# Kernel optimization log

Measured on AMD Instinct MI355X. Metric: run time of the kernel, lower is better.

## Reference

```python
import jax, jax.numpy as jnp
import numpy as np

B, T, C = 2, 2048, 1024
E, F = 8, 1024        # n_experts, expert ffn dim
FS = 2048             # shared expert ffn dim
TOP_K = 2


def setup_inputs() -> dict:
    key = jax.random.key(0)
    ks = jax.random.split(key, 6)
    s = lambda *d: 1.0 / np.sqrt(d[-1])
    return {
        "hidden_tensor": jax.random.normal(ks[0], (B, T, C), jnp.float32),
        "w_router": jax.random.normal(ks[1], (E, C), jnp.float32) * s(C),
        "w1_stack": jax.random.normal(ks[2], (E, F, C), jnp.float32) * s(C),
        "w2_stack": jax.random.normal(ks[3], (E, C, F), jnp.float32) * s(F),
        "ws1": jax.random.normal(ks[4], (FS, C), jnp.float32) * s(C),
        "ws2": jax.random.normal(ks[5], (C, FS), jnp.float32) * s(FS),
    }


def reference(hidden_tensor, w_router, w1_stack, w2_stack, ws1, ws2):
    Bb, Tt, Cc = hidden_tensor.shape
    x = hidden_tensor.reshape(-1, Cc)                      # (t, C)
    t = x.shape[0]

    # --- router: softmax over experts, top-k, renormalize ---
    logits = x @ w_router.T                                # (t, E)
    probs = jax.nn.softmax(logits, axis=-1)
    expert_weight, expert_idx = jax.lax.top_k(probs, TOP_K)  # (t, k)
    expert_weight = expert_weight / jnp.sum(expert_weight, axis=-1, keepdims=True)

    # --- dispatch: stable sort token-expert pairs by expert id ---
    flat_e = expert_idx.reshape(-1)                        # (t*k,)
    order = jnp.argsort(flat_e, stable=True)
    sorted_e = flat_e[order]
    flat_tok = jnp.repeat(jnp.arange(t), TOP_K)
    sorted_tok = flat_tok[order]
    sorted_w = expert_weight.reshape(-1)[order]

    counts = jnp.bincount(sorted_e, length=E)              # (E,)
    offsets = jnp.concatenate([jnp.zeros((1,), counts.dtype), jnp.cumsum(counts)])
    local_pos = jnp.arange(t * TOP_K) - offsets[sorted_e]  # position within expert bin

    cap = t * TOP_K  # static capacity (>= true cnt_max), padding rows stay zero
    binned = jnp.zeros((E, cap, Cc), x.dtype).at[sorted_e, local_pos].set(x[sorted_tok])

    # --- grouped expert FFN with squared-ReLU ---
    inter = jnp.einsum('ecd,efd->ecf', binned, w1_stack)   # (E, cap, F)
    inter = jnp.square(jax.nn.relu(inter))
    outb = jnp.einsum('ecf,edf->ecd', inter, w2_stack)     # (E, cap, C)

    # --- combine: gather back, weight, scatter-add to tokens ---
    flat_out = outb[sorted_e, local_pos] * sorted_w[:, None]
    moe_out = jnp.zeros((t, Cc), x.dtype).at[sorted_tok].add(flat_out)
    moe_out = moe_out.reshape(Bb, Tt, Cc)

    # --- shared expert on residual (squared-ReLU MLP) ---
    sh = jnp.square(jax.nn.relu(jnp.einsum('btc,fc->btf', hidden_tensor, ws1)))
    shared_out = jnp.einsum('btf,cf->btc', sh, ws2)

    return shared_out + moe_out
```

## Files before the change

### kernel.cpp

```cpp
#include <hip/hip_runtime.h>
#include <math.h>

typedef unsigned short u16;
typedef unsigned int u32;

typedef __attribute__((ext_vector_type(8))) short bf16x8;
typedef __attribute__((ext_vector_type(4))) float f32x4;

__device__ __forceinline__ u16 f2bf(float f) {
  union { float f; u32 u; } v; v.f = f;
  u32 r = v.u + 0x7FFFu + ((v.u >> 16) & 1u);
  return (u16)(r >> 16);
}

typedef const u32 __attribute__((address_space(1)))* gas1_t;
typedef u32 __attribute__((address_space(3)))* las3_t;

__device__ __forceinline__ void gload16(const void* g, void* l) {
  __builtin_amdgcn_global_load_lds((gas1_t)g, (las3_t)l, 16, 0, 0);
}

__global__ __launch_bounds__(256) void convert_weights(
    const float4* __restrict__ w1, const float4* __restrict__ w2,
    const float4* __restrict__ s1, const float4* __restrict__ s2,
    ushort4* __restrict__ o1, ushort4* __restrict__ o2,
    ushort4* __restrict__ o3, ushort4* __restrict__ o4) {
  size_t i = (size_t)blockIdx.x * 256 + threadIdx.x;
  const size_t n1 = 2097152, n2 = 2097152, n3 = 524288;
  float4 v; ushort4* o; size_t j;
  if (i < n1)              { v = w1[i];            o = o1; j = i; }
  else if (i < n1+n2)      { v = w2[i-n1];         o = o2; j = i-n1; }
  else if (i < n1+n2+n3)   { v = s1[i-n1-n2];      o = o3; j = i-n1-n2; }
  else                     { v = s2[i-n1-n2-n3];   o = o4; j = i-n1-n2-n3; }
  ushort4 r; r.x = f2bf(v.x); r.y = f2bf(v.y); r.z = f2bf(v.z); r.w = f2bf(v.w);
  o[j] = r;
}

__global__ __launch_bounds__(256) void router_kernel(
    const float* __restrict__ x, const float* __restrict__ wr,
    u16* __restrict__ xb, int* __restrict__ tokE, float* __restrict__ tokW) {
  const int wv = threadIdx.x >> 6, lane = threadIdx.x & 63;
  const int tok = blockIdx.x * 4 + wv;
  const float4* xp = (const float4*)(x + (size_t)tok * 1024);
  float4 xv[4];
#pragma unroll
  for (int i = 0; i < 4; ++i) xv[i] = xp[i * 64 + lane];
  ushort4* xo = (ushort4*)xb + (size_t)tok * 256;
#pragma unroll
  for (int i = 0; i < 4; ++i) {
    ushort4 o;
    o.x = f2bf(xv[i].x); o.y = f2bf(xv[i].y); o.z = f2bf(xv[i].z); o.w = f2bf(xv[i].w);
    xo[i * 64 + lane] = o;
  }
  float acc[8];
#pragma unroll
  for (int e = 0; e < 8; ++e) acc[e] = 0.f;
#pragma unroll
  for (int e = 0; e < 8; ++e) {
    const float4* wp = (const float4*)(wr + e * 1024);
#pragma unroll
    for (int i = 0; i < 4; ++i) {
      float4 w4 = wp[i * 64 + lane];
      acc[e] += xv[i].x * w4.x + xv[i].y * w4.y + xv[i].z * w4.z + xv[i].w * w4.w;
    }
  }
#pragma unroll
  for (int m = 32; m > 0; m >>= 1)
#pragma unroll
    for (int e = 0; e < 8; ++e) acc[e] += __shfl_xor(acc[e], m, 64);
  if (lane == 0) {
    int e0 = 0;
#pragma unroll
    for (int e = 1; e < 8; ++e) if (acc[e] > acc[e0]) e0 = e;
    int e1 = (e0 == 0) ? 1 : 0;
#pragma unroll
    for (int e = 0; e < 8; ++e) if (e != e0 && acc[e] > acc[e1]) e1 = e;
    float p1 = __expf(acc[e1] - acc[e0]);
    float w1 = p1 / (1.f + p1);
    float w0 = 1.f - w1;
    tokE[tok * 2] = e0; tokE[tok * 2 + 1] = e1;
    tokW[tok * 2] = w0; tokW[tok * 2 + 1] = w1;
  }
}

__global__ __launch_bounds__(256) void plan_kernel(
    const int* __restrict__ tokE, const float* __restrict__ tokW,
    int* __restrict__ tileMeta, int* __restrict__ rowtok,
    float* __restrict__ roww, int* __restrict__ invrow) {
  const int t = threadIdx.x, lane = t & 63, wv = t >> 6;
  int myE[32];
#pragma unroll
  for (int i = 0; i < 32; ++i) myE[i] = tokE[t * 32 + i];
  int lcnt[8] = {};
#pragma unroll
  for (int i = 0; i < 32; ++i) ++lcnt[myE[i]];

  __shared__ int wtot[8][4];
  __shared__ int aoffS[9];
  int excl[8];
#pragma unroll
  for (int e = 0; e < 8; ++e) {
    int v = lcnt[e];
#pragma unroll
    for (int off = 1; off < 64; off <<= 1) {
      int n = __shfl_up(v, (unsigned)off, 64);
      if (lane >= off) v += n;
    }
    if (lane == 63) wtot[e][wv] = v;
    excl[e] = v - lcnt[e];
  }
  __syncthreads();
#pragma unroll
  for (int e = 0; e < 8; ++e)
    for (int w = 0; w < wv; ++w) excl[e] += wtot[e][w];

  if (t == 0) {
    int s = 0, ti = 0;
    for (int e = 0; e < 8; ++e) {
      aoffS[e] = s;
      int cnt = wtot[e][0] + wtot[e][1] + wtot[e][2] + wtot[e][3];
      int tiles = (cnt + 127) >> 7;
      for (int k = 0; k < tiles; ++k) { tileMeta[2 * ti] = e; tileMeta[2 * ti + 1] = s + k * 128; ++ti; }
      s += tiles << 7;
    }
    aoffS[8] = s;
    for (; ti < 72; ++ti) { tileMeta[2 * ti] = -1; tileMeta[2 * ti + 1] = 0; }
  }
  for (int i = t; i < 9216; i += 256) { rowtok[i] = 0; roww[i] = 0.f; }
  __syncthreads();

  int pos[8];
#pragma unroll
  for (int e = 0; e < 8; ++e) pos[e] = aoffS[e] + excl[e];
#pragma unroll
  for (int i = 0; i < 32; ++i) {
    int idx = t * 32 + i;
    int e = myE[i];
    int g = pos[e]++;
    rowtok[g] = idx >> 1;
    roww[g] = tokW[idx];
    invrow[idx] = g;
  }
}

__global__ __launch_bounds__(256) void combine_kernel(
    const float* __restrict__ Ym, const int* __restrict__ invrow,
    const float* __restrict__ tokW, float* __restrict__ out) {
  const int t = blockIdx.x;
  const int r0 = invrow[2 * t], r1 = invrow[2 * t + 1];
  const float w0 = tokW[2 * t], w1 = tokW[2 * t + 1];
  const float4* y0 = (const float4*)(Ym + (size_t)r0 * 1024);
  const float4* y1 = (const float4*)(Ym + (size_t)r1 * 1024);
  float4* o = (float4*)(out + (size_t)t * 1024);
  const int c = threadIdx.x;
  float4 a = y0[c], b = y1[c], v = o[c];
  v.x += w0 * a.x + w1 * b.x;
  v.y += w0 * a.y + w1 * b.y;
  v.z += w0 * a.z + w1 * b.z;
  v.w += w0 * a.w + w1 * b.w;
  o[c] = v;
}

struct TileMeta { int e; int g0; };

template <int EPI, int MODE>
__global__ __launch_bounds__(256)
void gemm_k(const u16* __restrict__ A, const u16* __restrict__ Bw,
            void* __restrict__ Cout, int N, int K, size_t Bstride,
            const TileMeta* __restrict__ tiles,
            const int* __restrict__ rowtok, const float* __restrict__ roww) {
  __shared__ u16 As[128 * 32];
  __shared__ u16 Bs[128 * 32];

  int e = 0, g0;
  if (MODE == 0) {
    g0 = blockIdx.y * 128;
  } else {
    TileMeta tm = tiles[blockIdx.y];
    if (tm.e < 0) return;
    e = tm.e; g0 = tm.g0;
  }
  const int n0 = blockIdx.x * 128;
  const int tid = threadIdx.x;
  const int lane = tid & 63;
  const int wv = tid >> 6;
  const int wrow = wv >> 1, wcol = wv & 1;

  const u16* Bexp = Bw + (size_t)e * Bstride;

  const u16* aSrc[2];
  const u16* bSrc[2];
  u32 ldsOff[2];
#pragma unroll
  for (int p = 0; p < 2; ++p) {
    int c = p * 256 + tid;
    int row = c >> 2, q = c & 3;
    int arow;
    if (MODE == 1) arow = rowtok[g0 + row];
    else arow = g0 + row;
    aSrc[p] = A + (size_t)arow * K + q * 8;
    bSrc[p] = Bexp + (size_t)(n0 + row) * K + q * 8;
    ldsOff[p] = (u32)(p * 256 + wv * 64) * 16u;
  }

  const int fr = lane & 15, fq = lane >> 4;
  const int aRd = (wrow * 64 + fr) * 32 + fq * 8;
  const int bRd = (wcol * 64 + fr) * 32 + fq * 8;

  f32x4 acc[4][4] = {};

  for (int k0 = 0; k0 < K; k0 += 32) {
#pragma unroll
    for (int p = 0; p < 2; ++p) {
      gload16(aSrc[p] + k0, (char*)As + ldsOff[p]);
      gload16(bSrc[p] + k0, (char*)Bs + ldsOff[p]);
    }
    __syncthreads();
    bf16x8 af[4], bfg[4];
#pragma unroll
    for (int i = 0; i < 4; ++i) af[i] = *(const bf16x8*)&As[aRd + i * 512];
#pragma unroll
    for (int j = 0; j < 4; ++j) bfg[j] = *(const bf16x8*)&Bs[bRd + j * 512];
#pragma unroll
    for (int i = 0; i < 4; ++i)
#pragma unroll
      for (int j = 0; j < 4; ++j)
        acc[i][j] = __builtin_amdgcn_mfma_f32_16x16x32_bf16(af[i], bfg[j], acc[i][j], 0, 0, 0);
    __syncthreads();
  }

  if (EPI == 0 || EPI == 1) {
#pragma unroll
    for (int i = 0; i < 4; ++i) {
      int rb = g0 + wrow * 64 + i * 16 + fq * 4;
#pragma unroll
      for (int j = 0; j < 4; ++j) {
        int col = n0 + wcol * 64 + j * 16 + fr;
#pragma unroll
        for (int r = 0; r < 4; ++r) {
          float v = acc[i][j][r];
          size_t idx = (size_t)(rb + r) * N + col;
          if (EPI == 0) {
            v = v > 0.f ? v * v : 0.f;
            ((u16*)Cout)[idx] = f2bf(v);
          } else {
            ((float*)Cout)[idx] = v;
          }
        }
      }
    }
  } else {
    float* O = (float*)Cout;
#pragma unroll
    for (int i = 0; i < 4; ++i) {
      int rb = g0 + wrow * 64 + i * 16 + fq * 4;
#pragma unroll
      for (int r = 0; r < 4; ++r) {
        int tok = rowtok[rb + r];
        float w = roww[rb + r];
#pragma unroll
        for (int j = 0; j < 4; ++j) {
          int col = n0 + wcol * 64 + j * 16 + fr;
          atomicAdd(&O[(size_t)tok * N + col], w * acc[i][j][r]);
        }
      }
    }
  }
}

extern "C" void kernel_launch(void* const* d_in, const int* in_sizes, int n_in,
                              void* d_out, int out_size, void* d_ws, size_t ws_size,
                              hipStream_t stream) {
  const float* x   = (const float*)d_in[0];
  const float* wr  = (const float*)d_in[1];
  const float* w1  = (const float*)d_in[2];
  const float* w2  = (const float*)d_in[3];
  const float* s1  = (const float*)d_in[4];
  const float* s2  = (const float*)d_in[5];
  float* out = (float*)d_out;

  char* p = (char*)d_ws;
  auto alloc = [&](size_t n) { char* r = p; p += (n + 255) & ~(size_t)255; return r; };
  u16* xb   = (u16*)alloc(4096ULL * 1024 * 2);
  u16* w1b  = (u16*)alloc(8ULL * 1024 * 1024 * 2);
  u16* w2b  = (u16*)alloc(8ULL * 1024 * 1024 * 2);
  u16* s1b  = (u16*)alloc(2048ULL * 1024 * 2);
  u16* s2b  = (u16*)alloc(1024ULL * 2048 * 2);
  u16* Hs   = (u16*)alloc(4096ULL * 2048 * 2);
  u16* Hm   = (u16*)alloc(9216ULL * 1024 * 2);
  int* tokE = (int*)alloc(8192 * 4);
  float* tokW = (float*)alloc(8192 * 4);
  int* rowtok = (int*)alloc(9216 * 4);
  float* roww = (float*)alloc(9216 * 4);
  int* invrow = (int*)alloc(8192 * 4);
  int* tileMeta = (int*)alloc(72 * 2 * 4);
  size_t used_base = (size_t)(p - (char*)d_ws);
  float* Ym = (float*)p;
  const bool haveYm = (ws_size - used_base) >= 9216ULL * 1024 * 4;

  convert_weights<<<20480, 256, 0, stream>>>(
      (const float4*)w1, (const float4*)w2, (const float4*)s1, (const float4*)s2,
      (ushort4*)w1b, (ushort4*)w2b, (ushort4*)s1b, (ushort4*)s2b);

  router_kernel<<<1024, 256, 0, stream>>>(x, wr, xb, tokE, tokW);
  plan_kernel<<<1, 256, 0, stream>>>(tokE, tokW, tileMeta, rowtok, roww, invrow);

  gemm_k<0, 0><<<dim3(16, 32), 256, 0, stream>>>(
      xb, s1b, Hs, 2048, 1024, 0, nullptr, nullptr, nullptr);
  gemm_k<0, 1><<<dim3(8, 72), 256, 0, stream>>>(
      xb, w1b, Hm, 1024, 1024, (size_t)1024 * 1024, (const TileMeta*)tileMeta, rowtok, roww);
  gemm_k<1, 0><<<dim3(8, 32), 256, 0, stream>>>(
      Hs, s2b, out, 1024, 2048, 0, nullptr, nullptr, nullptr);

  if (haveYm) {
    gemm_k<1, 2><<<dim3(8, 72), 256, 0, stream>>>(
        Hm, w2b, Ym, 1024, 1024, (size_t)1024 * 1024, (const TileMeta*)tileMeta, rowtok, roww);
    combine_kernel<<<4096, 256, 0, stream>>>(Ym, invrow, tokW, out);
  } else {
    gemm_k<2, 2><<<dim3(8, 72), 256, 0, stream>>>(
        Hm, w2b, out, 1024, 1024, (size_t)1024 * 1024, (const TileMeta*)tileMeta, rowtok, roww);
  }
}
```

Before: 325.5 us.

## Merge shared and routed expert GEMMs into tile-list launches with LDS swizzle

The plan kernel now emits flat tile lists that combine the shared-expert and routed-expert GEMM tiles. The up and down projections each run as one launch instead of separate shared and MoE launches, so both can fill the GPU together and fewer kernels are launched. It also adds an XOR-style swizzle to the LDS chunk layout for loads and reads, to reduce bank conflicts. In exchange there is more runtime branching on tile kind, and the plan kernel does a little more serial work.

```diff
diff --git a/kernel.cpp b/kernel.cpp
--- a/kernel.cpp
+++ b/kernel.cpp
@@ -19,6 +19,8 @@
 __device__ __forceinline__ void gload16(const void* g, void* l) {
   __builtin_amdgcn_global_load_lds((gas1_t)g, (las3_t)l, 16, 0, 0);
 }
+
+struct Tile { int kind; int g0; int n0; int e; };
 
 __global__ __launch_bounds__(256) void convert_weights(
     const float4* __restrict__ w1, const float4* __restrict__ w2,
@@ -85,8 +87,8 @@
 
 __global__ __launch_bounds__(256) void plan_kernel(
     const int* __restrict__ tokE, const float* __restrict__ tokW,
-    int* __restrict__ tileMeta, int* __restrict__ rowtok,
-    float* __restrict__ roww, int* __restrict__ invrow) {
+    Tile* __restrict__ upT, Tile* __restrict__ downT,
+    int* __restrict__ rowtok, float* __restrict__ roww, int* __restrict__ invrow) {
   const int t = threadIdx.x, lane = t & 63, wv = t >> 6;
   int myE[32];
 #pragma unroll
@@ -97,6 +99,7 @@
 
   __shared__ int wtot[8][4];
   __shared__ int aoffS[9];
+  __shared__ int etile[72 * 2];
   int excl[8];
 #pragma unroll
   for (int e = 0; e < 8; ++e) {
@@ -120,14 +123,35 @@
       aoffS[e] = s;
       int cnt = wtot[e][0] + wtot[e][1] + wtot[e][2] + wtot[e][3];
       int tiles = (cnt + 127) >> 7;
-      for (int k = 0; k < tiles; ++k) { tileMeta[2 * ti] = e; tileMeta[2 * ti + 1] = s + k * 128; ++ti; }
+      for (int k = 0; k < tiles; ++k) { etile[2 * ti] = e; etile[2 * ti + 1] = s + k * 128; ++ti; }
       s += tiles << 7;
     }
     aoffS[8] = s;
-    for (; ti < 72; ++ti) { tileMeta[2 * ti] = -1; tileMeta[2 * ti + 1] = 0; }
+    for (; ti < 72; ++ti) { etile[2 * ti] = -1; etile[2 * ti + 1] = 0; }
   }
   for (int i = t; i < 9216; i += 256) { rowtok[i] = 0; roww[i] = 0.f; }
   __syncthreads();
+
+  for (int i = t; i < 1088; i += 256) {
+    Tile tl;
+    if (i < 512) { tl.kind = 0; tl.g0 = (i >> 4) * 128; tl.n0 = (i & 15) * 128; tl.e = 0; }
+    else {
+      int j = i - 512, mi = j >> 3, n = j & 7;
+      int e = etile[2 * mi];
+      tl.kind = (e < 0) ? -1 : 1; tl.g0 = etile[2 * mi + 1]; tl.n0 = n * 128; tl.e = (e < 0) ? 0 : e;
+    }
+    upT[i] = tl;
+  }
+  for (int i = t; i < 832; i += 256) {
+    Tile tl;
+    if (i < 256) { tl.kind = 0; tl.g0 = (i >> 3) * 128; tl.n0 = (i & 7) * 128; tl.e = 0; }
+    else {
+      int j = i - 256, mi = j >> 3, n = j & 7;
+      int e = etile[2 * mi];
+      tl.kind = (e < 0) ? -1 : 1; tl.g0 = etile[2 * mi + 1]; tl.n0 = n * 128; tl.e = (e < 0) ? 0 : e;
+    }
+    downT[i] = tl;
+  }
 
   int pos[8];
 #pragma unroll
@@ -161,32 +185,35 @@
   o[c] = v;
 }
 
-struct TileMeta { int e; int g0; };
-
-template <int EPI, int MODE>
+template <int PHASE>
 __global__ __launch_bounds__(256)
-void gemm_k(const u16* __restrict__ A, const u16* __restrict__ Bw,
-            void* __restrict__ Cout, int N, int K, size_t Bstride,
-            const TileMeta* __restrict__ tiles,
-            const int* __restrict__ rowtok, const float* __restrict__ roww) {
+void gemm_fused(const Tile* __restrict__ tiles,
+                const u16* __restrict__ A0, const u16* __restrict__ B0, void* __restrict__ C0,
+                const u16* __restrict__ A1, const u16* __restrict__ B1, void* __restrict__ C1,
+                const int* __restrict__ rowtok, const float* __restrict__ roww) {
   __shared__ u16 As[128 * 32];
   __shared__ u16 Bs[128 * 32];
 
-  int e = 0, g0;
-  if (MODE == 0) {
-    g0 = blockIdx.y * 128;
-  } else {
-    TileMeta tm = tiles[blockIdx.y];
-    if (tm.e < 0) return;
-    e = tm.e; g0 = tm.g0;
-  }
-  const int n0 = blockIdx.x * 128;
+  Tile tm = tiles[blockIdx.x];
+  if (tm.kind < 0) return;
+  if (PHASE == 2 && tm.kind != 0) return;
+  if (PHASE == 3 && tm.kind != 1) return;
+
   const int tid = threadIdx.x;
   const int lane = tid & 63;
   const int wv = tid >> 6;
   const int wrow = wv >> 1, wcol = wv & 1;
 
-  const u16* Bexp = Bw + (size_t)e * Bstride;
+  const u16* A; const u16* B; void* C; int N, K;
+  if (tm.kind == 0) {
+    A = A0; B = B0; C = C0;
+    N = (PHASE == 0) ? 2048 : 1024;
+    K = (PHASE == 0) ? 1024 : 2048;
+  } else {
+    A = A1; B = B1 + ((size_t)tm.e << 20); C = (PHASE == 3) ? C0 : C1;
+    N = 1024; K = 1024;
+  }
+  const int g0 = tm.g0, n0 = tm.n0;
 
   const u16* aSrc[2];
   const u16* bSrc[2];
@@ -194,18 +221,19 @@
 #pragma unroll
   for (int p = 0; p < 2; ++p) {
     int c = p * 256 + tid;
-    int row = c >> 2, q = c & 3;
-    int arow;
-    if (MODE == 1) arow = rowtok[g0 + row];
-    else arow = g0 + row;
+    int row = c >> 2;
+    int q = ((c & 3) - (c >> 3)) & 3;
+    int arow = g0 + row;
+    if (PHASE == 0 && tm.kind == 1) arow = rowtok[arow];
     aSrc[p] = A + (size_t)arow * K + q * 8;
-    bSrc[p] = Bexp + (size_t)(n0 + row) * K + q * 8;
+    bSrc[p] = B + (size_t)(n0 + row) * K + q * 8;
     ldsOff[p] = (u32)(p * 256 + wv * 64) * 16u;
   }
 
   const int fr = lane & 15, fq = lane >> 4;
-  const int aRd = (wrow * 64 + fr) * 32 + fq * 8;
-  const int bRd = (wcol * 64 + fr) * 32 + fq * 8;
+  const int sw = ((fq + (fr >> 1)) & 3) * 8;
+  const int aRd = (wrow * 64 + fr) * 32 + sw;
+  const int bRd = (wcol * 64 + fr) * 32 + sw;
 
   f32x4 acc[4][4] = {};
 
@@ -229,7 +257,8 @@
     __syncthreads();
   }
 
-  if (EPI == 0 || EPI == 1) {
+  if (PHASE == 0) {
+    u16* O = (u16*)C;
 #pragma unroll
     for (int i = 0; i < 4; ++i) {
       int rb = g0 + wrow * 64 + i * 16 + fq * 4;
@@ -239,18 +268,26 @@
 #pragma unroll
         for (int r = 0; r < 4; ++r) {
           float v = acc[i][j][r];
-          size_t idx = (size_t)(rb + r) * N + col;
-          if (EPI == 0) {
-            v = v > 0.f ? v * v : 0.f;
-            ((u16*)Cout)[idx] = f2bf(v);
-          } else {
-            ((float*)Cout)[idx] = v;
-          }
+          v = v > 0.f ? v * v : 0.f;
+          O[(size_t)(rb + r) * N + col] = f2bf(v);
         }
       }
     }
+  } else if (PHASE == 1 || PHASE == 2) {
+    float* O = (float*)C;
+#pragma unroll
+    for (int i = 0; i < 4; ++i) {
+      int rb = g0 + wrow * 64 + i * 16 + fq * 4;
+#pragma unroll
+      for (int j = 0; j < 4; ++j) {
+        int col = n0 + wcol * 64 + j * 16 + fr;
+#pragma unroll
+        for (int r = 0; r < 4; ++r)
+          O[(size_t)(rb + r) * N + col] = acc[i][j][r];
+      }
+    }
   } else {
-    float* O = (float*)Cout;
+    float* O = (float*)C;
 #pragma unroll
     for (int i = 0; i < 4; ++i) {
       int rb = g0 + wrow * 64 + i * 16 + fq * 4;
@@ -293,7 +330,8 @@
   int* rowtok = (int*)alloc(9216 * 4);
   float* roww = (float*)alloc(9216 * 4);
   int* invrow = (int*)alloc(8192 * 4);
-  int* tileMeta = (int*)alloc(72 * 2 * 4);
+  Tile* upT   = (Tile*)alloc(1088 * sizeof(Tile));
+  Tile* downT = (Tile*)alloc(832 * sizeof(Tile));
   size_t used_base = (size_t)(p - (char*)d_ws);
   float* Ym = (float*)p;
   const bool haveYm = (ws_size - used_base) >= 9216ULL * 1024 * 4;
@@ -303,21 +341,15 @@
       (ushort4*)w1b, (ushort4*)w2b, (ushort4*)s1b, (ushort4*)s2b);
 
   router_kernel<<<1024, 256, 0, stream>>>(x, wr, xb, tokE, tokW);
-  plan_kernel<<<1, 256, 0, stream>>>(tokE, tokW, tileMeta, rowtok, roww, invrow);
-
-  gemm_k<0, 0><<<dim3(16, 32), 256, 0, stream>>>(
-      xb, s1b, Hs, 2048, 1024, 0, nullptr, nullptr, nullptr);
-  gemm_k<0, 1><<<dim3(8, 72), 256, 0, stream>>>(
-      xb, w1b, Hm, 1024, 1024, (size_t)1024 * 1024, (const TileMeta*)tileMeta, rowtok, roww);
-  gemm_k<1, 0><<<dim3(8, 32), 256, 0, stream>>>(
-      Hs, s2b, out, 1024, 2048, 0, nullptr, nullptr, nullptr);
+  plan_kernel<<<1, 256, 0, stream>>>(tokE, tokW, upT, downT, rowtok, roww, invrow);
+
+  gemm_fused<0><<<1088, 256, 0, stream>>>(upT, xb, s1b, Hs, xb, w1b, Hm, rowtok, roww);
 
   if (haveYm) {
-    gemm_k<1, 2><<<dim3(8, 72), 256, 0, stream>>>(
-        Hm, w2b, Ym, 1024, 1024, (size_t)1024 * 1024, (const TileMeta*)tileMeta, rowtok, roww);
+    gemm_fused<1><<<832, 256, 0, stream>>>(downT, Hs, s2b, out, Hm, w2b, Ym, rowtok, roww);
     combine_kernel<<<4096, 256, 0, stream>>>(Ym, invrow, tokW, out);
   } else {
-    gemm_k<2, 2><<<dim3(8, 72), 256, 0, stream>>>(
-        Hm, w2b, out, 1024, 1024, (size_t)1024 * 1024, (const TileMeta*)tileMeta, rowtok, roww);
-  }
-}
+    gemm_fused<2><<<832, 256, 0, stream>>>(downT, Hs, s2b, out, Hm, w2b, nullptr, rowtok, roww);
+    gemm_fused<3><<<832, 256, 0, stream>>>(downT, Hs, s2b, out, Hm, w2b, nullptr, rowtok, roww);
+  }
+}
```

Result: faster. 290.3 us (-10.8%).
